# Kernel tuning notes

Measured on AMD Instinct MI355X. Metric: run time of the kernel, lower is better.

## Reference

```python
import jax, jax.numpy as jnp
import numpy as np

B, CQ, CC, COUT, H, W = 32, 256, 3, 256, 32, 32
INTER = CQ // 2
HC, WC = 224, 224
EPS = 1e-5


def setup_inputs() -> dict:
    key = jax.random.key(0)
    ks = jax.random.split(key, 12)
    s = lambda fan_in: 1.0 / np.sqrt(fan_in)
    return {
        "query_feat": jax.random.normal(ks[0], (B, CQ, H, W), jnp.float32),
        "context_feat": jax.random.normal(ks[1], (B, CC, HC, WC), jnp.float32),
        "Wq": jax.random.uniform(ks[2], (INTER, CQ), jnp.float32, -s(CQ), s(CQ)),
        "bq": jax.random.uniform(ks[3], (INTER,), jnp.float32, -s(CQ), s(CQ)),
        "Wk": jax.random.uniform(ks[4], (INTER, CC), jnp.float32, -s(CC), s(CC)),
        "bk": jax.random.uniform(ks[5], (INTER,), jnp.float32, -s(CC), s(CC)),
        "Wv": jax.random.uniform(ks[6], (CQ, CC), jnp.float32, -s(CC), s(CC)),
        "bv": jax.random.uniform(ks[7], (CQ,), jnp.float32, -s(CC), s(CC)),
        "Wp": jax.random.uniform(ks[8], (COUT, CQ), jnp.float32, -s(CQ), s(CQ)),
        "bp": jax.random.uniform(ks[9], (COUT,), jnp.float32, -s(CQ), s(CQ)),
        "gamma": jnp.ones((COUT,), jnp.float32),
        "beta": jnp.zeros((COUT,), jnp.float32),
    }


def _conv1x1(x, Wmat, b):
    # x: [B,Cin,H,W], Wmat: [Cout,Cin] -> [B,Cout,H,W]
    return jnp.einsum("oc,bchw->bohw", Wmat, x) + b[None, :, None, None]


def reference(query_feat, context_feat, Wq, bq, Wk, bk, Wv, bv, Wp, bp, gamma, beta):
    Bn, Cq, Hn, Wn = query_feat.shape
    HWn = Hn * Wn
    # bilinear resize, align_corners=False, no antialias (matches F.interpolate)
    ctx = jax.image.resize(context_feat, (Bn, context_feat.shape[1], Hn, Wn),
                           method="linear", antialias=False)
    q = _conv1x1(query_feat, Wq, bq).reshape(Bn, -1, HWn)   # [B,inter,HW]
    k = _conv1x1(ctx, Wk, bk).reshape(Bn, -1, HWn)          # [B,inter,HW]
    v = _conv1x1(ctx, Wv, bv).reshape(Bn, Cq, HWn)          # [B,Cq,HW]
    scores = jnp.einsum("bci,bcj->bij", q, k)               # [B,HW,HW]
    probs = jax.nn.softmax(scores, axis=-1)
    # attended_v[b,c,i] = sum_j v[b,c,j] * probs[b,i,j]
    attended = jnp.einsum("bcj,bij->bci", v, probs).reshape(Bn, Cq, Hn, Wn)
    fused = _conv1x1(query_feat + attended, Wp, bp)         # [B,Cout,H,W]
    # GroupNorm with 1 group: normalize over (C,H,W) per sample
    mu = jnp.mean(fused, axis=(1, 2, 3), keepdims=True)
    var = jnp.var(fused, axis=(1, 2, 3), keepdims=True)
    normed = (fused - mu) * jax.lax.rsqrt(var + EPS)
    return normed * gamma[None, :, None, None] + beta[None, :, None, None]
```

## Files before the change

kernel.cpp:

```cpp
#include <hip/hip_runtime.h>
#include <hip/hip_bf16.h>

#define WS_M4    0
#define WS_M0    1024
#define WS_G4    1056
#define WS_BSUM  2080
#define WS_BSSQ  2112
#define WS_BAR   2144
#define WS_WPB   2176
#define WS_CTX   34944

typedef __attribute__((ext_vector_type(8))) short short8;
typedef __attribute__((ext_vector_type(4))) float floatx4;

__device__ inline unsigned short f2bf(float x) {
    unsigned u = __float_as_uint(x);
    return (unsigned short)((u + 0x7FFFu + ((u >> 16) & 1u)) >> 16);
}

__global__ __launch_bounds__(256) void sca_pre(
    const float* __restrict__ Wq, const float* __restrict__ bq,
    const float* __restrict__ Wk, const float* __restrict__ bk,
    const float* __restrict__ Wv, const float* __restrict__ bv,
    const float* __restrict__ Wp, const float* __restrict__ bp,
    const float* __restrict__ ctxin, float* __restrict__ ws)
{
    int tid = threadIdx.x;
    int blk = blockIdx.x;
    if (blk < 4) {
        __shared__ float WkL[384];
        __shared__ float bqL[128];
        __shared__ float redM[4][64][3];
        int o0 = blk << 6;
        if (tid < 128) bqL[tid] = bq[tid];
        for (int idx = tid; idx < 384; idx += 256) WkL[idx] = Wk[idx];
        __syncthreads();
        int o64 = tid & 63, cg = tid >> 6;
        float m0v = 0.f, m1v = 0.f, m2v = 0.f;
        for (int c0 = cg * 32; c0 < cg * 32 + 32; c0 += 16) {
            float q[16];
#pragma unroll
            for (int j = 0; j < 16; ++j) q[j] = Wq[(c0 + j) * 256 + o0 + o64];
#pragma unroll
            for (int j = 0; j < 16; ++j) {
                int c = c0 + j;
                m0v = fmaf(WkL[c * 3 + 0], q[j], m0v);
                m1v = fmaf(WkL[c * 3 + 1], q[j], m1v);
                m2v = fmaf(WkL[c * 3 + 2], q[j], m2v);
            }
        }
        redM[cg][o64][0] = m0v; redM[cg][o64][1] = m1v; redM[cg][o64][2] = m2v;
        __syncthreads();
        if (tid < 64) {
            float r0 = redM[0][tid][0] + redM[1][tid][0] + redM[2][tid][0] + redM[3][tid][0];
            float r1 = redM[0][tid][1] + redM[1][tid][1] + redM[2][tid][1] + redM[3][tid][1];
            float r2 = redM[0][tid][2] + redM[1][tid][2] + redM[2][tid][2] + redM[3][tid][2];
            ((float4*)(ws + WS_M4))[o0 + tid] = make_float4(r0, r1, r2, 0.f);
        }
        if (blk == 0) {
            if (tid < 3) {
                float s = 0.f;
                for (int c = 0; c < 128; ++c) s = fmaf(WkL[c * 3 + tid], bqL[c], s);
                ws[WS_M0 + tid] = s;
            }
            if (tid < 65) ws[WS_BSUM + tid] = 0.f;
        }
    } else if (blk < 36) {
        __shared__ float WvL[768];
        __shared__ float bvL[256];
        for (int idx = tid; idx < 768; idx += 256) WvL[idx] = Wv[idx];
        bvL[tid] = bv[tid];
        __syncthreads();
        int idx = (blk - 4) * 2048 + tid * 8;
        int o = idx >> 8;
        int kt = (tid & 31) >> 2, quad = tid & 3;
        const float4* s = (const float4*)(Wp + idx);
        float4 x0 = s[0], x1 = s[1];
        uint4 v;
        v.x = (unsigned)f2bf(x0.x) | ((unsigned)f2bf(x0.y) << 16);
        v.y = (unsigned)f2bf(x0.z) | ((unsigned)f2bf(x0.w) << 16);
        v.z = (unsigned)f2bf(x1.x) | ((unsigned)f2bf(x1.y) << 16);
        v.w = (unsigned)f2bf(x1.z) | ((unsigned)f2bf(x1.w) << 16);
        int slot = (((o >> 4) * 8 + kt) * 64) + quad * 16 + (o & 15);
        ((uint4*)((unsigned short*)(ws + WS_WPB)))[slot] = v;
        int c0 = idx & 255;
        float xv[8] = {x0.x, x0.y, x0.z, x0.w, x1.x, x1.y, x1.z, x1.w};
        float g0 = 0.f, g1 = 0.f, g2 = 0.f, gb = 0.f;
#pragma unroll
        for (int j = 0; j < 8; ++j) {
            int c = c0 + j;
            g0 = fmaf(xv[j], WvL[c * 3 + 0], g0);
            g1 = fmaf(xv[j], WvL[c * 3 + 1], g1);
            g2 = fmaf(xv[j], WvL[c * 3 + 2], g2);
            gb = fmaf(xv[j], bvL[c], gb);
        }
#pragma unroll
        for (int off = 1; off < 32; off <<= 1) {
            g0 += __shfl_xor(g0, off);
            g1 += __shfl_xor(g1, off);
            g2 += __shfl_xor(g2, off);
            gb += __shfl_xor(gb, off);
        }
        if ((tid & 31) == 0)
            ((float4*)(ws + WS_G4))[o] = make_float4(g0, g1, g2, gb + bp[o]);
    } else {
        int g = (blk - 36) * 256 + tid;
        int b = g >> 10, j = g & 1023;
        int y = j >> 5, x = j & 31;
        const float* src = ctxin + (size_t)b * 150528;
        int p = (7 * y + 3) * 224 + (7 * x + 3);
        ((float4*)(ws + WS_CTX))[g] =
            make_float4(src[p], src[p + 50176], src[p + 100352], 0.f);
    }
}

__global__ __launch_bounds__(512, 2) void sca_mega(const float* __restrict__ Q,
                                                   float* __restrict__ ws,
                                                   const float* __restrict__ gamma,
                                                   const float* __restrict__ beta,
                                                   float* __restrict__ out)
{
    __shared__ float4 cs4[1024];
    __shared__ float4 Ms4[256];
    __shared__ uint4 QL[2048];
    __shared__ float red[8][64][13];
    __shared__ float4 av4[256];
    __shared__ float4 cps[256];
    __shared__ float sred[18];

    int tid = threadIdx.x;
    int blk = blockIdx.x;
    int b  = blk >> 3;
    int oh = (blk >> 2) & 1;
    int i0 = (blk & 3) << 8;
    int lane = tid & 63, w = tid >> 6;
    int m = lane & 15, quad = lane >> 4;

    {
        const float4* cg4 = ((const float4*)(ws + WS_CTX)) + ((size_t)b << 10);
        cs4[tid] = cg4[tid];
        cs4[512 + tid] = cg4[512 + tid];
        if (tid < 256) Ms4[tid] = ((const float4*)(ws + WS_M4))[tid];
    }
    __syncthreads();

    const short8* Apack = (const short8*)((const unsigned short*)(ws + WS_WPB));
    int otile = oh * 8 + w;

    floatx4 acc[16] = {};
    float ap[12] = {};
    const float* Qbase = Q + ((size_t)b << 18) + i0 + (lane << 2);

    for (int c = 0; c < 4; ++c) {
        float4 qv[8];
#pragma unroll
        for (int s = 0; s < 8; ++s)
            qv[s] = *(const float4*)(Qbase + ((size_t)(c * 64 + w * 8 + s) << 10));
        if (c > 0) __syncthreads();
#pragma unroll
        for (int s = 0; s < 8; ++s) {
            float4 mv = Ms4[c * 64 + w * 8 + s];
#pragma unroll
            for (int e = 0; e < 4; ++e) {
                float qe = ((const float*)&qv[s])[e];
                ap[0 + e] = fmaf(mv.x, qe, ap[0 + e]);
                ap[4 + e] = fmaf(mv.y, qe, ap[4 + e]);
                ap[8 + e] = fmaf(mv.z, qe, ap[8 + e]);
            }
        }
#pragma unroll
        for (int e = 0; e < 4; ++e) {
            uint4 v;
            v.x = (unsigned)f2bf(((const float*)&qv[0])[e]) | ((unsigned)f2bf(((const float*)&qv[1])[e]) << 16);
            v.y = (unsigned)f2bf(((const float*)&qv[2])[e]) | ((unsigned)f2bf(((const float*)&qv[3])[e]) << 16);
            v.z = (unsigned)f2bf(((const float*)&qv[4])[e]) | ((unsigned)f2bf(((const float*)&qv[5])[e]) << 16);
            v.w = (unsigned)f2bf(((const float*)&qv[6])[e]) | ((unsigned)f2bf(((const float*)&qv[7])[e]) << 16);
            int i = (lane << 2) + e;
            int gs = w ^ (i & 7) ^ ((i >> 2) & 7);
            QL[i * 8 + gs] = v;
        }
        __syncthreads();
#pragma unroll
        for (int kk = 0; kk < 2; ++kk) {
            short8 af = Apack[((otile * 8) + (c * 2 + kk)) * 64 + lane];
#pragma unroll
            for (int it = 0; it < 16; ++it) {
                int i = it * 16 + m;
                int g = kk * 4 + quad;
                int gs = g ^ (i & 7) ^ ((i >> 2) & 7);
                short8 bf = ((const short8*)QL)[i * 8 + gs];
                acc[it] = __builtin_amdgcn_mfma_f32_16x16x32_bf16(
                    af, bf, acc[it], 0, 0, 0);
            }
        }
    }

#pragma unroll
    for (int c2 = 0; c2 < 12; ++c2) red[w][lane][c2] = ap[c2];
    __syncthreads();
    if (tid < 256) {
        int iq = tid >> 2, e = tid & 3;
        float r0 = ws[WS_M0 + 0], r1 = ws[WS_M0 + 1], r2 = ws[WS_M0 + 2];
#pragma unroll
        for (int wv = 0; wv < 8; ++wv) {
            r0 += red[wv][iq][0 + e];
            r1 += red[wv][iq][4 + e];
            r2 += red[wv][iq][8 + e];
        }
        av4[tid] = make_float4(r0, r1, r2, 0.f);
    }
    __syncthreads();

    {
        int sl = tid & 7, qg = tid >> 3;
        float4 a0 = av4[qg], a1 = av4[qg + 64], a2 = av4[qg + 128], a3 = av4[qg + 192];
        float sh0 = 6.0f * (fabsf(a0.x) + fabsf(a0.y) + fabsf(a0.z));
        float sh1 = 6.0f * (fabsf(a1.x) + fabsf(a1.y) + fabsf(a1.z));
        float sh2 = 6.0f * (fabsf(a2.x) + fabsf(a2.y) + fabsf(a2.z));
        float sh3 = 6.0f * (fabsf(a3.x) + fabsf(a3.y) + fabsf(a3.z));
        float d0=0.f,x0=0.f,y0=0.f,z0=0.f, d1=0.f,x1=0.f,y1=0.f,z1=0.f;
        float d2=0.f,x2=0.f,y2=0.f,z2=0.f, d3=0.f,x3=0.f,y3=0.f,z3=0.f;
#pragma unroll 4
        for (int jj = 0; jj < 128; ++jj) {
            float4 cv = cs4[(jj << 3) + sl];
            float sc, e;
            sc = fmaf(a0.x, cv.x, fmaf(a0.y, cv.y, a0.z * cv.z));
            e = __expf(sc - sh0);
            d0 += e; x0 = fmaf(e, cv.x, x0); y0 = fmaf(e, cv.y, y0); z0 = fmaf(e, cv.z, z0);
            sc = fmaf(a1.x, cv.x, fmaf(a1.y, cv.y, a1.z * cv.z));
            e = __expf(sc - sh1);
            d1 += e; x1 = fmaf(e, cv.x, x1); y1 = fmaf(e, cv.y, y1); z1 = fmaf(e, cv.z, z1);
            sc = fmaf(a2.x, cv.x, fmaf(a2.y, cv.y, a2.z * cv.z));
            e = __expf(sc - sh2);
            d2 += e; x2 = fmaf(e, cv.x, x2); y2 = fmaf(e, cv.y, y2); z2 = fmaf(e, cv.z, z2);
            sc = fmaf(a3.x, cv.x, fmaf(a3.y, cv.y, a3.z * cv.z));
            e = __expf(sc - sh3);
            d3 += e; x3 = fmaf(e, cv.x, x3); y3 = fmaf(e, cv.y, y3); z3 = fmaf(e, cv.z, z3);
        }
#pragma unroll
        for (int off = 1; off < 8; off <<= 1) {
            d0 += __shfl_xor(d0, off); x0 += __shfl_xor(x0, off); y0 += __shfl_xor(y0, off); z0 += __shfl_xor(z0, off);
            d1 += __shfl_xor(d1, off); x1 += __shfl_xor(x1, off); y1 += __shfl_xor(y1, off); z1 += __shfl_xor(z1, off);
            d2 += __shfl_xor(d2, off); x2 += __shfl_xor(x2, off); y2 += __shfl_xor(y2, off); z2 += __shfl_xor(z2, off);
            d3 += __shfl_xor(d3, off); x3 += __shfl_xor(x3, off); y3 += __shfl_xor(y3, off); z3 += __shfl_xor(z3, off);
        }
        if (sl == 0) {
            float i0v = 1.0f / d0, i1v = 1.0f / d1, i2v = 1.0f / d2, i3v = 1.0f / d3;
            cps[qg      ] = make_float4(x0 * i0v, y0 * i0v, z0 * i0v, 0.f);
            cps[qg +  64] = make_float4(x1 * i1v, y1 * i1v, z1 * i1v, 0.f);
            cps[qg + 128] = make_float4(x2 * i2v, y2 * i2v, z2 * i2v, 0.f);
            cps[qg + 192] = make_float4(x3 * i3v, y3 * i3v, z3 * i3v, 0.f);
        }
    }
    __syncthreads();

    const floatx4* G4 = (const floatx4*)(ws + WS_G4);
    floatx4 gv[4];
    float gaw[4], btw[4];
#pragma unroll
    for (int r = 0; r < 4; ++r) {
        int o = oh * 128 + w * 16 + quad * 4 + r;
        gv[r] = G4[o];
        gaw[r] = gamma[o];
        btw[r] = beta[o];
    }
    float lsum = 0.f, lssq = 0.f;
#pragma unroll
    for (int it = 0; it < 16; ++it) {
        float4 cp = cps[it * 16 + m];
#pragma unroll
        for (int r = 0; r < 4; ++r) {
            float v = acc[it][r]
                    + gv[r][0] * cp.x + gv[r][1] * cp.y + gv[r][2] * cp.z + gv[r][3];
            acc[it][r] = v;
            lsum += v; lssq = fmaf(v, v, lssq);
        }
    }
#pragma unroll
    for (int off = 32; off > 0; off >>= 1) {
        lsum += __shfl_down(lsum, off);
        lssq += __shfl_down(lssq, off);
    }
    if (lane == 0) { sred[w] = lsum; sred[8 + w] = lssq; }
    __syncthreads();

    if (tid == 0) {
        float s = 0.f, q2 = 0.f;
#pragma unroll
        for (int j = 0; j < 8; ++j) { s += sred[j]; q2 += sred[8 + j]; }
        atomicAdd(ws + WS_BSUM + b, s);
        atomicAdd(ws + WS_BSSQ + b, q2);
        __threadfence();
        int* bar = (int*)(ws + WS_BAR);
        atomicAdd(bar, 1);
        while (atomicAdd(bar, 0) < 256) __builtin_amdgcn_s_sleep(2);
        sred[16] = atomicAdd(ws + WS_BSUM + b, 0.0f);
        sred[17] = atomicAdd(ws + WS_BSSQ + b, 0.0f);
    }
    __syncthreads();

    const float inv_n = 1.0f / 262144.0f;
    float mean = sred[16] * inv_n;
    float var  = fmaf(sred[17], inv_n, -mean * mean);
    float rs = rsqrtf(var + 1e-5f);
    float gm[4], gb2[4];
#pragma unroll
    for (int r = 0; r < 4; ++r) {
        gm[r] = gaw[r] * rs;
        gb2[r] = fmaf(-mean, gm[r], btw[r]);
    }
#pragma unroll
    for (int it = 0; it < 16; ++it) {
#pragma unroll
        for (int r = 0; r < 4; ++r) {
            int o = oh * 128 + w * 16 + quad * 4 + r;
            out[(((size_t)(b * 256 + o)) << 10) + i0 + it * 16 + m] =
                fmaf(acc[it][r], gm[r], gb2[r]);
        }
    }
}

extern "C" void kernel_launch(void* const* d_in, const int* in_sizes, int n_in,
                              void* d_out, int out_size, void* d_ws, size_t ws_size,
                              hipStream_t stream)
{
    const float* Q     = (const float*)d_in[0];
    const float* ctxf  = (const float*)d_in[1];
    const float* Wq    = (const float*)d_in[2];
    const float* bq    = (const float*)d_in[3];
    const float* Wk    = (const float*)d_in[4];
    const float* bk    = (const float*)d_in[5];
    const float* Wv    = (const float*)d_in[6];
    const float* bv    = (const float*)d_in[7];
    const float* Wp    = (const float*)d_in[8];
    const float* bp    = (const float*)d_in[9];
    const float* gamma = (const float*)d_in[10];
    const float* beta  = (const float*)d_in[11];
    float* ws  = (float*)d_ws;
    float* out = (float*)d_out;

    sca_pre <<<164, 256, 0, stream>>>(Wq, bq, Wk, bk, Wv, bv, Wp, bp, ctxf, ws);
    sca_mega<<<256, 512, 0, stream>>>(Q, ws, gamma, beta, out);
}
```

Measured before the change: 165.1 us.

## Repartition mega kernel to 1024-thread blocks covering all output channels

Each block now covers all 256 output channels for 128 query positions, using 16 waves instead of splitting channels across two blocks of 8 waves. The softmax-over-context work is no longer computed twice per position across channel halves, each thread handles fewer positions, and the next Q chunk is loaded while the current one is processed, with the bf16 staging buffer double-buffered. In exchange, blocks are larger and need more registers and LDS each, which may limit occupancy, and the spin-wait grid barrier still needs all 256 blocks resident at once.

```diff
diff --git a/kernel.cpp b/kernel.cpp
--- a/kernel.cpp
+++ b/kernel.cpp
@@ -114,81 +114,80 @@
     }
 }
 
-__global__ __launch_bounds__(512, 2) void sca_mega(const float* __restrict__ Q,
-                                                   float* __restrict__ ws,
-                                                   const float* __restrict__ gamma,
-                                                   const float* __restrict__ beta,
-                                                   float* __restrict__ out)
+__global__ __launch_bounds__(1024, 4) void sca_mega(const float* __restrict__ Q,
+                                                    float* __restrict__ ws,
+                                                    const float* __restrict__ gamma,
+                                                    const float* __restrict__ beta,
+                                                    float* __restrict__ out)
 {
     __shared__ float4 cs4[1024];
     __shared__ float4 Ms4[256];
     __shared__ uint4 QL[2048];
-    __shared__ float red[8][64][13];
-    __shared__ float4 av4[256];
-    __shared__ float4 cps[256];
-    __shared__ float sred[18];
+    __shared__ float red[16][64][7];
+    __shared__ float4 av4[128];
+    __shared__ float4 cps[128];
+    __shared__ float sred[34];
 
     int tid = threadIdx.x;
     int blk = blockIdx.x;
     int b  = blk >> 3;
-    int oh = (blk >> 2) & 1;
-    int i0 = (blk & 3) << 8;
+    int i0 = (blk & 7) << 7;
     int lane = tid & 63, w = tid >> 6;
     int m = lane & 15, quad = lane >> 4;
 
+    const float* Qbase = Q + ((size_t)b << 18) + i0 + (lane << 1);
+    float2 qv[4];
+#pragma unroll
+    for (int s = 0; s < 4; ++s)
+        qv[s] = *(const float2*)(Qbase + ((size_t)(w * 4 + s) << 10));
     {
         const float4* cg4 = ((const float4*)(ws + WS_CTX)) + ((size_t)b << 10);
         cs4[tid] = cg4[tid];
-        cs4[512 + tid] = cg4[512 + tid];
         if (tid < 256) Ms4[tid] = ((const float4*)(ws + WS_M4))[tid];
     }
     __syncthreads();
 
     const short8* Apack = (const short8*)((const unsigned short*)(ws + WS_WPB));
-    int otile = oh * 8 + w;
-
-    floatx4 acc[16] = {};
-    float ap[12] = {};
-    const float* Qbase = Q + ((size_t)b << 18) + i0 + (lane << 2);
+    floatx4 acc[8] = {};
+    float ap[6] = {};
 
     for (int c = 0; c < 4; ++c) {
-        float4 qv[8];
-#pragma unroll
-        for (int s = 0; s < 8; ++s)
-            qv[s] = *(const float4*)(Qbase + ((size_t)(c * 64 + w * 8 + s) << 10));
-        if (c > 0) __syncthreads();
-#pragma unroll
-        for (int s = 0; s < 8; ++s) {
-            float4 mv = Ms4[c * 64 + w * 8 + s];
-#pragma unroll
-            for (int e = 0; e < 4; ++e) {
-                float qe = ((const float*)&qv[s])[e];
-                ap[0 + e] = fmaf(mv.x, qe, ap[0 + e]);
-                ap[4 + e] = fmaf(mv.y, qe, ap[4 + e]);
-                ap[8 + e] = fmaf(mv.z, qe, ap[8 + e]);
-            }
-        }
-#pragma unroll
-        for (int e = 0; e < 4; ++e) {
-            uint4 v;
-            v.x = (unsigned)f2bf(((const float*)&qv[0])[e]) | ((unsigned)f2bf(((const float*)&qv[1])[e]) << 16);
-            v.y = (unsigned)f2bf(((const float*)&qv[2])[e]) | ((unsigned)f2bf(((const float*)&qv[3])[e]) << 16);
-            v.z = (unsigned)f2bf(((const float*)&qv[4])[e]) | ((unsigned)f2bf(((const float*)&qv[5])[e]) << 16);
-            v.w = (unsigned)f2bf(((const float*)&qv[6])[e]) | ((unsigned)f2bf(((const float*)&qv[7])[e]) << 16);
-            int i = (lane << 2) + e;
-            int gs = w ^ (i & 7) ^ ((i >> 2) & 7);
-            QL[i * 8 + gs] = v;
+#pragma unroll
+        for (int s = 0; s < 4; ++s) {
+            float4 mv = Ms4[c * 64 + w * 4 + s];
+            ap[0] = fmaf(mv.x, qv[s].x, ap[0]); ap[1] = fmaf(mv.x, qv[s].y, ap[1]);
+            ap[2] = fmaf(mv.y, qv[s].x, ap[2]); ap[3] = fmaf(mv.y, qv[s].y, ap[3]);
+            ap[4] = fmaf(mv.z, qv[s].x, ap[4]); ap[5] = fmaf(mv.z, qv[s].y, ap[5]);
+        }
+        unsigned lo0 = (unsigned)f2bf(qv[0].x) | ((unsigned)f2bf(qv[1].x) << 16);
+        unsigned hi0 = (unsigned)f2bf(qv[2].x) | ((unsigned)f2bf(qv[3].x) << 16);
+        unsigned lo1 = (unsigned)f2bf(qv[0].y) | ((unsigned)f2bf(qv[1].y) << 16);
+        unsigned hi1 = (unsigned)f2bf(qv[2].y) | ((unsigned)f2bf(qv[3].y) << 16);
+        {
+            uint2* QB = (uint2*)(QL + (c & 1) * 1024);
+            int i = lane << 1;
+            int gs = (w >> 1) ^ (i & 7) ^ ((i >> 2) & 7);
+            QB[(i * 8 + gs) * 2 + (w & 1)] = make_uint2(lo0, hi0);
+            i |= 1;
+            gs = (w >> 1) ^ (i & 7) ^ ((i >> 2) & 7);
+            QB[(i * 8 + gs) * 2 + (w & 1)] = make_uint2(lo1, hi1);
+        }
+        if (c < 3) {
+#pragma unroll
+            for (int s = 0; s < 4; ++s)
+                qv[s] = *(const float2*)(Qbase + ((size_t)((c + 1) * 64 + w * 4 + s) << 10));
         }
         __syncthreads();
+        const short8* QBs = (const short8*)(QL + (c & 1) * 1024);
 #pragma unroll
         for (int kk = 0; kk < 2; ++kk) {
-            short8 af = Apack[((otile * 8) + (c * 2 + kk)) * 64 + lane];
-#pragma unroll
-            for (int it = 0; it < 16; ++it) {
+            short8 af = Apack[(w * 8 + c * 2 + kk) * 64 + lane];
+#pragma unroll
+            for (int it = 0; it < 8; ++it) {
                 int i = it * 16 + m;
                 int g = kk * 4 + quad;
                 int gs = g ^ (i & 7) ^ ((i >> 2) & 7);
-                short8 bf = ((const short8*)QL)[i * 8 + gs];
+                short8 bf = QBs[i * 8 + gs];
                 acc[it] = __builtin_amdgcn_mfma_f32_16x16x32_bf16(
                     af, bf, acc[it], 0, 0, 0);
             }
@@ -196,16 +195,16 @@
     }
 
 #pragma unroll
-    for (int c2 = 0; c2 < 12; ++c2) red[w][lane][c2] = ap[c2];
-    __syncthreads();
-    if (tid < 256) {
-        int iq = tid >> 2, e = tid & 3;
+    for (int j = 0; j < 6; ++j) red[w][lane][j] = ap[j];
+    __syncthreads();
+    if (tid < 128) {
+        int ln = tid >> 1, e = tid & 1;
         float r0 = ws[WS_M0 + 0], r1 = ws[WS_M0 + 1], r2 = ws[WS_M0 + 2];
 #pragma unroll
-        for (int wv = 0; wv < 8; ++wv) {
-            r0 += red[wv][iq][0 + e];
-            r1 += red[wv][iq][4 + e];
-            r2 += red[wv][iq][8 + e];
+        for (int wv = 0; wv < 16; ++wv) {
+            r0 += red[wv][ln][0 + e];
+            r1 += red[wv][ln][2 + e];
+            r2 += red[wv][ln][4 + e];
         }
         av4[tid] = make_float4(r0, r1, r2, 0.f);
     }
@@ -213,43 +212,26 @@
 
     {
         int sl = tid & 7, qg = tid >> 3;
-        float4 a0 = av4[qg], a1 = av4[qg + 64], a2 = av4[qg + 128], a3 = av4[qg + 192];
-        float sh0 = 6.0f * (fabsf(a0.x) + fabsf(a0.y) + fabsf(a0.z));
-        float sh1 = 6.0f * (fabsf(a1.x) + fabsf(a1.y) + fabsf(a1.z));
-        float sh2 = 6.0f * (fabsf(a2.x) + fabsf(a2.y) + fabsf(a2.z));
-        float sh3 = 6.0f * (fabsf(a3.x) + fabsf(a3.y) + fabsf(a3.z));
-        float d0=0.f,x0=0.f,y0=0.f,z0=0.f, d1=0.f,x1=0.f,y1=0.f,z1=0.f;
-        float d2=0.f,x2=0.f,y2=0.f,z2=0.f, d3=0.f,x3=0.f,y3=0.f,z3=0.f;
+        float4 a = av4[qg];
+        float sh = 6.0f * (fabsf(a.x) + fabsf(a.y) + fabsf(a.z));
+        float d = 0.f, s0 = 0.f, s1 = 0.f, s2 = 0.f;
 #pragma unroll 4
         for (int jj = 0; jj < 128; ++jj) {
             float4 cv = cs4[(jj << 3) + sl];
-            float sc, e;
-            sc = fmaf(a0.x, cv.x, fmaf(a0.y, cv.y, a0.z * cv.z));
-            e = __expf(sc - sh0);
-            d0 += e; x0 = fmaf(e, cv.x, x0); y0 = fmaf(e, cv.y, y0); z0 = fmaf(e, cv.z, z0);
-            sc = fmaf(a1.x, cv.x, fmaf(a1.y, cv.y, a1.z * cv.z));
-            e = __expf(sc - sh1);
-            d1 += e; x1 = fmaf(e, cv.x, x1); y1 = fmaf(e, cv.y, y1); z1 = fmaf(e, cv.z, z1);
-            sc = fmaf(a2.x, cv.x, fmaf(a2.y, cv.y, a2.z * cv.z));
-            e = __expf(sc - sh2);
-            d2 += e; x2 = fmaf(e, cv.x, x2); y2 = fmaf(e, cv.y, y2); z2 = fmaf(e, cv.z, z2);
-            sc = fmaf(a3.x, cv.x, fmaf(a3.y, cv.y, a3.z * cv.z));
-            e = __expf(sc - sh3);
-            d3 += e; x3 = fmaf(e, cv.x, x3); y3 = fmaf(e, cv.y, y3); z3 = fmaf(e, cv.z, z3);
-        }
-#pragma unroll
-        for (int off = 1; off < 8; off <<= 1) {
-            d0 += __shfl_xor(d0, off); x0 += __shfl_xor(x0, off); y0 += __shfl_xor(y0, off); z0 += __shfl_xor(z0, off);
-            d1 += __shfl_xor(d1, off); x1 += __shfl_xor(x1, off); y1 += __shfl_xor(y1, off); z1 += __shfl_xor(z1, off);
-            d2 += __shfl_xor(d2, off); x2 += __shfl_xor(x2, off); y2 += __shfl_xor(y2, off); z2 += __shfl_xor(z2, off);
-            d3 += __shfl_xor(d3, off); x3 += __shfl_xor(x3, off); y3 += __shfl_xor(y3, off); z3 += __shfl_xor(z3, off);
-        }
+            float sc = fmaf(a.x, cv.x, fmaf(a.y, cv.y, a.z * cv.z));
+            float e = __expf(sc - sh);
+            d += e;
+            s0 = fmaf(e, cv.x, s0);
+            s1 = fmaf(e, cv.y, s1);
+            s2 = fmaf(e, cv.z, s2);
+        }
+        d  += __shfl_xor(d, 1);  d  += __shfl_xor(d, 2);  d  += __shfl_xor(d, 4);
+        s0 += __shfl_xor(s0, 1); s0 += __shfl_xor(s0, 2); s0 += __shfl_xor(s0, 4);
+        s1 += __shfl_xor(s1, 1); s1 += __shfl_xor(s1, 2); s1 += __shfl_xor(s1, 4);
+        s2 += __shfl_xor(s2, 1); s2 += __shfl_xor(s2, 2); s2 += __shfl_xor(s2, 4);
         if (sl == 0) {
-            float i0v = 1.0f / d0, i1v = 1.0f / d1, i2v = 1.0f / d2, i3v = 1.0f / d3;
-            cps[qg      ] = make_float4(x0 * i0v, y0 * i0v, z0 * i0v, 0.f);
-            cps[qg +  64] = make_float4(x1 * i1v, y1 * i1v, z1 * i1v, 0.f);
-            cps[qg + 128] = make_float4(x2 * i2v, y2 * i2v, z2 * i2v, 0.f);
-            cps[qg + 192] = make_float4(x3 * i3v, y3 * i3v, z3 * i3v, 0.f);
+            float inv = 1.0f / d;
+            cps[qg] = make_float4(s0 * inv, s1 * inv, s2 * inv, 0.f);
         }
     }
     __syncthreads();
@@ -259,14 +241,14 @@
     float gaw[4], btw[4];
 #pragma unroll
     for (int r = 0; r < 4; ++r) {
-        int o = oh * 128 + w * 16 + quad * 4 + r;
+        int o = w * 16 + quad * 4 + r;
         gv[r] = G4[o];
         gaw[r] = gamma[o];
         btw[r] = beta[o];
     }
     float lsum = 0.f, lssq = 0.f;
 #pragma unroll
-    for (int it = 0; it < 16; ++it) {
+    for (int it = 0; it < 8; ++it) {
         float4 cp = cps[it * 16 + m];
 #pragma unroll
         for (int r = 0; r < 4; ++r) {
@@ -281,27 +263,27 @@
         lsum += __shfl_down(lsum, off);
         lssq += __shfl_down(lssq, off);
     }
-    if (lane == 0) { sred[w] = lsum; sred[8 + w] = lssq; }
+    if (lane == 0) { sred[w] = lsum; sred[16 + w] = lssq; }
     __syncthreads();
 
     if (tid == 0) {
         float s = 0.f, q2 = 0.f;
 #pragma unroll
-        for (int j = 0; j < 8; ++j) { s += sred[j]; q2 += sred[8 + j]; }
+        for (int j = 0; j < 16; ++j) { s += sred[j]; q2 += sred[16 + j]; }
         atomicAdd(ws + WS_BSUM + b, s);
         atomicAdd(ws + WS_BSSQ + b, q2);
         __threadfence();
         int* bar = (int*)(ws + WS_BAR);
         atomicAdd(bar, 1);
         while (atomicAdd(bar, 0) < 256) __builtin_amdgcn_s_sleep(2);
-        sred[16] = atomicAdd(ws + WS_BSUM + b, 0.0f);
-        sred[17] = atomicAdd(ws + WS_BSSQ + b, 0.0f);
+        sred[32] = atomicAdd(ws + WS_BSUM + b, 0.0f);
+        sred[33] = atomicAdd(ws + WS_BSSQ + b, 0.0f);
     }
     __syncthreads();
 
     const float inv_n = 1.0f / 262144.0f;
-    float mean = sred[16] * inv_n;
-    float var  = fmaf(sred[17], inv_n, -mean * mean);
+    float mean = sred[32] * inv_n;
+    float var  = fmaf(sred[33], inv_n, -mean * mean);
     float rs = rsqrtf(var + 1e-5f);
     float gm[4], gb2[4];
 #pragma unroll
@@ -310,10 +292,10 @@
         gb2[r] = fmaf(-mean, gm[r], btw[r]);
     }
 #pragma unroll
-    for (int it = 0; it < 16; ++it) {
+    for (int it = 0; it < 8; ++it) {
 #pragma unroll
         for (int r = 0; r < 4; ++r) {
-            int o = oh * 128 + w * 16 + quad * 4 + r;
+            int o = w * 16 + quad * 4 + r;
             out[(((size_t)(b * 256 + o)) << 10) + i0 + it * 16 + m] =
                 fmaf(acc[it][r], gm[r], gb2[r]);
         }
@@ -340,5 +322,5 @@
     float* out = (float*)d_out;
 
     sca_pre <<<164, 256, 0, stream>>>(Wq, bq, Wk, bk, Wv, bv, Wp, bp, ctxf, ws);
-    sca_mega<<<256, 512, 0, stream>>>(Q, ws, gamma, beta, out);
+    sca_mega<<<256, 1024, 0, stream>>>(Q, ws, gamma, beta, out);
 }
```

After: 148.2 us. -10.3%, faster.
